# Kernel tuning notes

Hardware: AMD Instinct MI355X
Metric: run time of the kernel (lower is better)

The kernel has to match this reference:

```python
import jax, jax.numpy as jnp
import numpy as np

N = 8192
D = 256


def setup_inputs() -> dict:
    key = jax.random.key(0)
    ks = jax.random.split(key, 10)
    s = 1.0 / np.sqrt(D)
    inp = {
        "embeddings": jax.random.normal(ks[0], (N, D), dtype=jnp.float32),
        "adjacency": jax.random.randint(ks[1], (N, N), 0, 2, dtype=jnp.int32),
        "Wq": jax.random.uniform(ks[2], (D, D), jnp.float32, -s, s),
        "bq": jax.random.uniform(ks[3], (D,), jnp.float32, -s, s),
        "Wk": jax.random.uniform(ks[4], (D, D), jnp.float32, -s, s),
        "bk": jax.random.uniform(ks[5], (D,), jnp.float32, -s, s),
        "Wv": jax.random.uniform(ks[6], (D, D), jnp.float32, -s, s),
        "bv": jax.random.uniform(ks[7], (D,), jnp.float32, -s, s),
        "Wo": jax.random.uniform(ks[8], (D, D), jnp.float32, -s, s),
        "bo": jax.random.uniform(ks[9], (D,), jnp.float32, -s, s),
    }
    return inp


def reference(embeddings, adjacency, Wq, bq, Wk, bk, Wv, bv, Wo, bo):
    # Q/K/V projections (torch Linear: x @ W.T + b)
    Q = embeddings @ Wq.T + bq            # [N, D]
    K = embeddings @ Wk.T + bk            # [N, D]
    V = embeddings @ Wv.T + bv            # [N, D]
    scale = 1.0 / jnp.sqrt(jnp.asarray(D, dtype=embeddings.dtype))
    scores = (Q @ K.T) * scale            # [N, N]
    scores = jnp.where(adjacency == 0, jnp.asarray(-1e9, scores.dtype), scores)
    attn = jax.nn.softmax(scores, axis=-1)  # dropout is identity in eval mode
    context = attn @ V                    # [N, D]
    return context @ Wo.T + bo
```

## Files before the change

kernel.cpp:

```cpp
#include <hip/hip_runtime.h>
#include <hip/hip_bf16.h>


#define LOG2E 1.44269504088896340736f
#define MASKVAL -3.0e38f
#define MINIT   -1.0e38f

using f32x4 = __attribute__((ext_vector_type(4))) float;
using s16x8 = __attribute__((ext_vector_type(8))) short;
using s16x4 = __attribute__((ext_vector_type(4))) short;

__device__ __forceinline__ void gl_lds16(void* l, const void* g) {
  __builtin_amdgcn_global_load_lds(
      (const __attribute__((address_space(1))) void*)g,
      (__attribute__((address_space(3))) void*)l, 16, 0, 0);
}

__device__ __forceinline__ short f2bf(float x) {
  union { float f; unsigned u; } v; v.f = x;
  unsigned r = v.u + 0x7fffu + ((v.u >> 16) & 1u);
  return (short)(r >> 16);
}

__device__ __forceinline__ s16x8 cvt_frag(f32x4 a, f32x4 b) {
  s16x8 r;
  r[0]=f2bf(a[0]); r[1]=f2bf(a[1]); r[2]=f2bf(a[2]); r[3]=f2bf(a[3]);
  r[4]=f2bf(b[0]); r[5]=f2bf(b[1]); r[6]=f2bf(b[2]); r[7]=f2bf(b[3]);
  return r;
}

__device__ __forceinline__ f32x4 mfma16(s16x8 a, s16x8 b, f32x4 c) {
  return __builtin_amdgcn_mfma_f32_16x16x32_bf16(a, b, c, 0, 0, 0);
}

template<bool A_BF16, bool OUT_BF16, bool TRANS_OUT>
__global__ __launch_bounds__(256, 4)
void proj_kernel(const void* __restrict__ Ap, const float* __restrict__ W,
                 const float* __restrict__ bias, void* __restrict__ outp,
                 float scale)
{
  __shared__ __align__(16) char ldsA[A_BF16 ? 8192 : 16384];
  __shared__ __align__(16) char ldsB[16384];
  const int tid = threadIdx.x;
  const int lane = tid & 63, w = tid >> 6;
  const int wr = w >> 1, wc = w & 1;
  const int l15 = lane & 15, lhi = lane >> 4;
  const int m0 = blockIdx.x * 64, n0 = blockIdx.y * 64;
  const char* Ab = (const char*)Ap;
  const char* Wb = (const char*)W;

  f32x4 acc[2][2] = {};

  for (int k0 = 0; k0 < 256; k0 += 64) {
    if (A_BF16) {
#pragma unroll
      for (int i = 0; i < 2; ++i) {
        int o = tid * 16 + i * 4096;
        int row = o >> 7, inrow = o & 127;
        gl_lds16(ldsA + o, Ab + (size_t)(m0 + row) * 512 + k0 * 2 + (inrow ^ ((row & 7) << 4)));
      }
    } else {
#pragma unroll
      for (int i = 0; i < 4; ++i) {
        int o = tid * 16 + i * 4096;
        int row = o >> 8, inrow = o & 255;
        gl_lds16(ldsA + o, Ab + (size_t)(m0 + row) * 1024 + k0 * 4 + (inrow ^ ((row & 7) << 4)));
      }
    }
#pragma unroll
    for (int i = 0; i < 4; ++i) {
      int o = tid * 16 + i * 4096;
      int row = o >> 8, inrow = o & 255;
      gl_lds16(ldsB + o, Wb + (size_t)(n0 + row) * 1024 + k0 * 4 + (inrow ^ ((row & 7) << 4)));
    }
    __syncthreads();

#pragma unroll
    for (int ks = 0; ks < 2; ++ks) {
      s16x8 af[2], bfr[2];
#pragma unroll
      for (int m = 0; m < 2; ++m) {
        int row = wr * 32 + m * 16 + l15;
        if (A_BF16) {
          int c = ks * 64 + lhi * 16;
          af[m] = *(const s16x8*)(ldsA + row * 128 + (c ^ ((row & 7) << 4)));
        } else {
          int c = ks * 128 + lhi * 32;
          f32x4 lo = *(const f32x4*)(ldsA + row * 256 + (c ^ ((row & 7) << 4)));
          f32x4 hi = *(const f32x4*)(ldsA + row * 256 + ((c + 16) ^ ((row & 7) << 4)));
          af[m] = cvt_frag(lo, hi);
        }
      }
#pragma unroll
      for (int n = 0; n < 2; ++n) {
        int row = wc * 32 + n * 16 + l15;
        int c = ks * 128 + lhi * 32;
        f32x4 lo = *(const f32x4*)(ldsB + row * 256 + (c ^ ((row & 7) << 4)));
        f32x4 hi = *(const f32x4*)(ldsB + row * 256 + ((c + 16) ^ ((row & 7) << 4)));
        bfr[n] = cvt_frag(lo, hi);
      }
#pragma unroll
      for (int m = 0; m < 2; ++m)
#pragma unroll
        for (int n = 0; n < 2; ++n)
          acc[m][n] = mfma16(af[m], bfr[n], acc[m][n]);
    }
    __syncthreads();
  }

#pragma unroll
  for (int n = 0; n < 2; ++n) {
    int col = n0 + wc * 32 + n * 16 + l15;
    float bv = bias[col];
#pragma unroll
    for (int m = 0; m < 2; ++m) {
      int rbase = m0 + wr * 32 + m * 16 + lhi * 4;
      if (TRANS_OUT) {
        s16x4 pk;
#pragma unroll
        for (int r = 0; r < 4; ++r) pk[r] = f2bf((acc[m][n][r] + bv) * scale);
        *(s16x4*)((unsigned short*)outp + (size_t)col * 8192 + rbase) = pk;
      } else if (OUT_BF16) {
#pragma unroll
        for (int r = 0; r < 4; ++r)
          ((unsigned short*)outp)[(size_t)(rbase + r) * 256 + col] =
              (unsigned short)f2bf((acc[m][n][r] + bv) * scale);
      } else {
#pragma unroll
        for (int r = 0; r < 4; ++r)
          ((float*)outp)[(size_t)(rbase + r) * 256 + col] = (acc[m][n][r] + bv) * scale;
      }
    }
  }
}

template<int SPLIT, bool DIRECT, bool PACC_BF16>
__global__ __launch_bounds__(256, 2)
void attn_kernel(const unsigned short* __restrict__ Qb, const char* __restrict__ Kb,
                 const char* __restrict__ VbT, const int* __restrict__ adj,
                 void* __restrict__ pacc, float* __restrict__ pm,
                 float* __restrict__ pl, unsigned short* __restrict__ CX)
{
  __shared__ __align__(16) char ldsK[32768];
  __shared__ __align__(16) char ldsV[32768];
  __shared__ __align__(16) char ldsP[16384];
  const int tid = threadIdx.x, lane = tid & 63, w = tid >> 6;
  const int l15 = lane & 15, lhi = lane >> 4;
  const int qt = blockIdx.x / SPLIT, sp = blockIdx.x % SPLIT;
  const int q0 = qt * 128 + w * 32;
  char* myP = ldsP + w * 4096;
  const int kv_begin = sp * (8192 / SPLIT);
  const int NT = 8192 / SPLIT / 64;

  s16x8 qf[2][8];
#pragma unroll
  for (int f = 0; f < 2; ++f) {
    const unsigned short* qp = Qb + (size_t)(q0 + f * 16 + l15) * 256 + lhi * 8;
#pragma unroll
    for (int ks = 0; ks < 8; ++ks) qf[f][ks] = *(const s16x8*)(qp + ks * 32);
  }

  f32x4 ctx[2][16] = {};
  float m_run[2][4], l_run[2][4];
#pragma unroll
  for (int f = 0; f < 2; ++f)
#pragma unroll
    for (int r = 0; r < 4; ++r) { m_run[f][r] = MINIT; l_run[f][r] = 0.f; }

  for (int t = 0; t < NT; ++t) {
    const int kv0 = kv_begin + t * 64;

    {
      const char* kg = Kb + (size_t)kv0 * 512;
#pragma unroll
      for (int i = 0; i < 8; ++i) {
        int o = tid * 16 + i * 4096;
        int row = o >> 9, inrow = o & 511;
        gl_lds16(ldsK + o, kg + row * 512 + (inrow ^ ((row & 7) << 4)));
      }
#pragma unroll
      for (int i = 0; i < 8; ++i) {
        int o = tid * 16 + i * 4096;
        int row = o >> 7, inrow = o & 127;
        gl_lds16(ldsV + o, VbT + (size_t)row * 16384 + (size_t)kv0 * 2 + (inrow ^ ((row & 7) << 4)));
      }
    }

    int am[2][4][4];
#pragma unroll
    for (int f = 0; f < 2; ++f) {
      const int* ap = adj + (size_t)(q0 + f * 16 + lhi * 4) * 8192 + kv0 + l15;
#pragma unroll
      for (int r = 0; r < 4; ++r)
#pragma unroll
        for (int cg = 0; cg < 4; ++cg)
          am[f][r][cg] = ap[(size_t)r * 8192 + cg * 16];
    }

    __syncthreads();

    f32x4 sacc[2][4] = {};
    __builtin_amdgcn_s_setprio(1);
#pragma unroll
    for (int ks = 0; ks < 8; ++ks)
#pragma unroll
      for (int cg = 0; cg < 4; ++cg) {
        int row = cg * 16 + l15;
        s16x8 kf = *(const s16x8*)(ldsK + row * 512 + ((ks * 64 + lhi * 16) ^ ((row & 7) << 4)));
        sacc[0][cg] = mfma16(qf[0][ks], kf, sacc[0][cg]);
        sacc[1][cg] = mfma16(qf[1][ks], kf, sacc[1][cg]);
      }
    __builtin_amdgcn_s_setprio(0);

#pragma unroll
    for (int f = 0; f < 2; ++f)
#pragma unroll
      for (int r = 0; r < 4; ++r)
#pragma unroll
        for (int cg = 0; cg < 4; ++cg)
          if (am[f][r][cg] == 0) sacc[f][cg][r] = MASKVAL;

    float tmax[2][4];
#pragma unroll
    for (int f = 0; f < 2; ++f)
#pragma unroll
      for (int r = 0; r < 4; ++r)
        tmax[f][r] = fmaxf(fmaxf(sacc[f][0][r], sacc[f][1][r]),
                           fmaxf(sacc[f][2][r], sacc[f][3][r]));
#pragma unroll
    for (int mk = 1; mk <= 8; mk <<= 1)
#pragma unroll
      for (int f = 0; f < 2; ++f)
#pragma unroll
        for (int r = 0; r < 4; ++r)
          tmax[f][r] = fmaxf(tmax[f][r], __shfl_xor(tmax[f][r], mk, 64));

    float need = MASKVAL;
#pragma unroll
    for (int f = 0; f < 2; ++f)
#pragma unroll
      for (int r = 0; r < 4; ++r)
        need = fmaxf(need, tmax[f][r] - m_run[f][r]);
    if (!__all(need <= 8.0f)) {
#pragma unroll
      for (int f = 0; f < 2; ++f) {
        f32x4 fv;
#pragma unroll
        for (int r = 0; r < 4; ++r) {
          float mnew = fmaxf(m_run[f][r], tmax[f][r]);
          float fs = __builtin_amdgcn_exp2f((m_run[f][r] - mnew) * LOG2E);
          m_run[f][r] = mnew; l_run[f][r] *= fs; fv[r] = fs;
        }
#pragma unroll
        for (int dm = 0; dm < 16; ++dm) ctx[f][dm] *= fv;
      }
    }

#pragma unroll
    for (int f = 0; f < 2; ++f)
#pragma unroll
      for (int cg = 0; cg < 4; ++cg)
#pragma unroll
        for (int r = 0; r < 4; ++r) {
          float p = __builtin_amdgcn_exp2f((sacc[f][cg][r] - m_run[f][r]) * LOG2E);
          l_run[f][r] += p;
          int row = f * 16 + lhi * 4 + r;
          int cb = (cg * 16 + l15) * 2;
          *(short*)(myP + row * 128 + (cb ^ ((row & 7) << 4))) = f2bf(p);
        }

    __builtin_amdgcn_s_setprio(1);
#pragma unroll
    for (int ks = 0; ks < 2; ++ks) {
      s16x8 pf[2];
#pragma unroll
      for (int f = 0; f < 2; ++f) {
        int prow = f * 16 + l15;
        pf[f] = *(const s16x8*)(myP + prow * 128 + (((ks * 32 + lhi * 8) * 2) ^ ((prow & 7) << 4)));
      }
#pragma unroll
      for (int dm = 0; dm < 16; ++dm) {
        int vrow = dm * 16 + l15;
        s16x8 vf = *(const s16x8*)(ldsV + vrow * 128 + (((ks * 32 + lhi * 8) * 2) ^ ((vrow & 7) << 4)));
        ctx[0][dm] = mfma16(pf[0], vf, ctx[0][dm]);
        ctx[1][dm] = mfma16(pf[1], vf, ctx[1][dm]);
      }
    }
    __builtin_amdgcn_s_setprio(0);
    __syncthreads();
  }

#pragma unroll
  for (int mk = 1; mk <= 8; mk <<= 1)
#pragma unroll
    for (int f = 0; f < 2; ++f)
#pragma unroll
      for (int r = 0; r < 4; ++r)
        l_run[f][r] += __shfl_xor(l_run[f][r], mk, 64);

  if (DIRECT) {
#pragma unroll
    for (int f = 0; f < 2; ++f)
#pragma unroll
      for (int r = 0; r < 4; ++r) {
        float inv = 1.0f / l_run[f][r];
        size_t rowb = (size_t)(q0 + f * 16 + lhi * 4 + r) * 256 + l15;
#pragma unroll
        for (int dm = 0; dm < 16; ++dm)
          CX[rowb + dm * 16] = (unsigned short)f2bf(ctx[f][dm][r] * inv);
      }
  } else {
#pragma unroll
    for (int f = 0; f < 2; ++f)
#pragma unroll
      for (int r = 0; r < 4; ++r) {
        size_t rowb = (size_t)sp * 8192 * 256 +
                      (size_t)(q0 + f * 16 + lhi * 4 + r) * 256 + l15;
        if (PACC_BF16) {
#pragma unroll
          for (int dm = 0; dm < 16; ++dm)
            ((unsigned short*)pacc)[rowb + dm * 16] = (unsigned short)f2bf(ctx[f][dm][r]);
        } else {
#pragma unroll
          for (int dm = 0; dm < 16; ++dm)
            ((float*)pacc)[rowb + dm * 16] = ctx[f][dm][r];
        }
      }
    if (l15 == 0) {
#pragma unroll
      for (int f = 0; f < 2; ++f)
#pragma unroll
        for (int r = 0; r < 4; ++r) {
          pm[(size_t)sp * 8192 + q0 + f * 16 + lhi * 4 + r] = m_run[f][r];
          pl[(size_t)sp * 8192 + q0 + f * 16 + lhi * 4 + r] = l_run[f][r];
        }
    }
  }
}

template<bool PACC_BF16>
__global__ __launch_bounds__(256)
void combine_kernel(const void* __restrict__ pacc, const float* __restrict__ pm,
                    const float* __restrict__ pl, unsigned short* __restrict__ cx)
{
  const int row = blockIdx.x;
  const int d = threadIdx.x;
  float M = MINIT;
#pragma unroll
  for (int s = 0; s < 8; ++s) M = fmaxf(M, pm[s * 8192 + row]);
  float L = 0.f, v = 0.f;
#pragma unroll
  for (int s = 0; s < 8; ++s) {
    float ws = __builtin_amdgcn_exp2f((pm[s * 8192 + row] - M) * LOG2E);
    L += ws * pl[s * 8192 + row];
    size_t idx = (size_t)s * 8192 * 256 + (size_t)row * 256 + d;
    float pv;
    if (PACC_BF16) {
      union { unsigned u; float f; } c; c.u = (unsigned)((const unsigned short*)pacc)[idx] << 16;
      pv = c.f;
    } else {
      pv = ((const float*)pacc)[idx];
    }
    v += ws * pv;
  }
  cx[(size_t)row * 256 + d] = (unsigned short)f2bf(v / L);
}

extern "C" void kernel_launch(void* const* d_in, const int* in_sizes, int n_in,
                              void* d_out, int out_size, void* d_ws, size_t ws_size,
                              hipStream_t stream)
{
  const float* E  = (const float*)d_in[0];
  const int*  adj = (const int*)d_in[1];
  const float* Wq = (const float*)d_in[2];
  const float* bq = (const float*)d_in[3];
  const float* Wk = (const float*)d_in[4];
  const float* bk = (const float*)d_in[5];
  const float* Wv = (const float*)d_in[6];
  const float* bv = (const float*)d_in[7];
  const float* Wo = (const float*)d_in[8];
  const float* bo = (const float*)d_in[9];

  char* ws = (char*)d_ws;
  unsigned short* Qb = (unsigned short*)(ws);
  unsigned short* Kb = (unsigned short*)(ws + ((size_t)4 << 20));
  unsigned short* VT = (unsigned short*)(ws + ((size_t)8 << 20));
  unsigned short* CX = (unsigned short*)(ws + ((size_t)12 << 20));
  char* pacc = ws + ((size_t)16 << 20);

  dim3 g(128, 4), b(256);
  hipLaunchKernelGGL((proj_kernel<false, true, false>), g, b, 0, stream, E, Wq, bq, Qb, 0.0625f);
  hipLaunchKernelGGL((proj_kernel<false, true, false>), g, b, 0, stream, E, Wk, bk, Kb, 1.0f);
  hipLaunchKernelGGL((proj_kernel<false, true, true>),  g, b, 0, stream, E, Wv, bv, VT, 1.0f);

  const size_t PACC_F32_BYTES  = (size_t)8 * 8192 * 256 * 4;
  const size_t PACC_BF16_BYTES = (size_t)8 * 8192 * 256 * 2;
  const size_t PMPL = (size_t)8 * 8192 * 4;
  const size_t NEED_F32  = ((size_t)16 << 20) + PACC_F32_BYTES + 2 * PMPL;
  const size_t NEED_BF16 = ((size_t)16 << 20) + PACC_BF16_BYTES + 2 * PMPL;

  if (ws_size >= NEED_F32) {
    float* pm = (float*)(pacc + PACC_F32_BYTES);
    float* pl = pm + 8 * 8192;
    hipLaunchKernelGGL((attn_kernel<8, false, false>), dim3(512), b, 0, stream,
                       Qb, (const char*)Kb, (const char*)VT, adj, pacc, pm, pl, CX);
    hipLaunchKernelGGL((combine_kernel<false>), dim3(8192), b, 0, stream, pacc, pm, pl, CX);
  } else if (ws_size >= NEED_BF16) {
    float* pm = (float*)(pacc + PACC_BF16_BYTES);
    float* pl = pm + 8 * 8192;
    hipLaunchKernelGGL((attn_kernel<8, false, true>), dim3(512), b, 0, stream,
                       Qb, (const char*)Kb, (const char*)VT, adj, pacc, pm, pl, CX);
    hipLaunchKernelGGL((combine_kernel<true>), dim3(8192), b, 0, stream, pacc, pm, pl, CX);
  } else {
    float* pm = (float*)pacc; float* pl = pm + 8192;
    hipLaunchKernelGGL((attn_kernel<1, true, false>), dim3(64), b, 0, stream,
                       Qb, (const char*)Kb, (const char*)VT, adj, pacc, pm, pl, CX);
  }
  hipLaunchKernelGGL((proj_kernel<true, false, false>), g, b, 0, stream, CX, Wo, bo, d_out, 1.0f);
}
```

Baseline: 675.8 us.

## Repack adjacency to bitmask and fuse Q/K/V projections into one kernel

Adds a pre-pass that compresses the int32 adjacency matrix into a per-row bitmask using wave ballots. The attention kernel then reads one 64-bit word per row per tile instead of 16 scattered ints per lane, which cuts the mask traffic inside the attention loop. The three Q/K/V projections are also fused into one kernel that loads the embedding tile once and reuses it for all three weight matrices. The cost is an extra full read of the 256MB adjacency in the repack pass, plus more LDS use and lower occupancy in the fused projection.

```diff
diff --git a/kernel.cpp b/kernel.cpp
--- a/kernel.cpp
+++ b/kernel.cpp
@@ -33,45 +33,135 @@
   return __builtin_amdgcn_mfma_f32_16x16x32_bf16(a, b, c, 0, 0, 0);
 }
 
-template<bool A_BF16, bool OUT_BF16, bool TRANS_OUT>
+__global__ __launch_bounds__(256)
+void repack_kernel(const int* __restrict__ adj, unsigned long long* __restrict__ bm)
+{
+  const int row = blockIdx.x;
+  const int w = threadIdx.x >> 6, lane = threadIdx.x & 63;
+  const int* src = adj + (size_t)row * 8192 + w * 2048;
+  unsigned long long* dst = bm + (size_t)row * 128 + w * 32;
+#pragma unroll 4
+  for (int it = 0; it < 32; ++it) {
+    int x = src[it * 64 + lane];
+    unsigned long long b = __ballot(x != 0);
+    if (lane == 0) dst[it] = b;
+  }
+}
+
+__global__ __launch_bounds__(256, 2)
+void qkv_kernel(const float* __restrict__ E,
+                const float* __restrict__ Wq, const float* __restrict__ bq,
+                const float* __restrict__ Wk, const float* __restrict__ bk,
+                const float* __restrict__ Wv, const float* __restrict__ bv,
+                unsigned short* __restrict__ Qb, unsigned short* __restrict__ Kb,
+                unsigned short* __restrict__ VT)
+{
+  __shared__ __align__(16) char ldsA[16384];
+  __shared__ __align__(16) char ldsB[3][16384];
+  const int tid = threadIdx.x;
+  const int lane = tid & 63, w = tid >> 6;
+  const int wr = w >> 1, wc = w & 1;
+  const int l15 = lane & 15, lhi = lane >> 4;
+  const int m0 = blockIdx.x * 64, n0 = blockIdx.y * 64;
+  const float* Ws[3] = {Wq, Wk, Wv};
+
+  f32x4 acc[3][2][2] = {};
+
+  for (int k0 = 0; k0 < 256; k0 += 64) {
+#pragma unroll
+    for (int i = 0; i < 4; ++i) {
+      int o = tid * 16 + i * 4096;
+      int row = o >> 8, inrow = o & 255;
+      gl_lds16(ldsA + o, (const char*)E + (size_t)(m0 + row) * 1024 + k0 * 4 + (inrow ^ ((row & 7) << 4)));
+    }
+#pragma unroll
+    for (int mtx = 0; mtx < 3; ++mtx)
+#pragma unroll
+      for (int i = 0; i < 4; ++i) {
+        int o = tid * 16 + i * 4096;
+        int row = o >> 8, inrow = o & 255;
+        gl_lds16(ldsB[mtx] + o, (const char*)Ws[mtx] + (size_t)(n0 + row) * 1024 + k0 * 4 + (inrow ^ ((row & 7) << 4)));
+      }
+    __syncthreads();
+
+#pragma unroll
+    for (int ks = 0; ks < 2; ++ks) {
+      s16x8 af[2];
+#pragma unroll
+      for (int m = 0; m < 2; ++m) {
+        int row = wr * 32 + m * 16 + l15;
+        int c = ks * 128 + lhi * 32;
+        f32x4 lo = *(const f32x4*)(ldsA + row * 256 + (c ^ ((row & 7) << 4)));
+        f32x4 hi = *(const f32x4*)(ldsA + row * 256 + ((c + 16) ^ ((row & 7) << 4)));
+        af[m] = cvt_frag(lo, hi);
+      }
+#pragma unroll
+      for (int mtx = 0; mtx < 3; ++mtx) {
+        s16x8 bfr[2];
+#pragma unroll
+        for (int n = 0; n < 2; ++n) {
+          int row = wc * 32 + n * 16 + l15;
+          int c = ks * 128 + lhi * 32;
+          f32x4 lo = *(const f32x4*)(ldsB[mtx] + row * 256 + (c ^ ((row & 7) << 4)));
+          f32x4 hi = *(const f32x4*)(ldsB[mtx] + row * 256 + ((c + 16) ^ ((row & 7) << 4)));
+          bfr[n] = cvt_frag(lo, hi);
+        }
+#pragma unroll
+        for (int m = 0; m < 2; ++m)
+#pragma unroll
+          for (int n = 0; n < 2; ++n)
+            acc[mtx][m][n] = mfma16(af[m], bfr[n], acc[mtx][m][n]);
+      }
+    }
+    __syncthreads();
+  }
+
+#pragma unroll
+  for (int n = 0; n < 2; ++n) {
+    int col = n0 + wc * 32 + n * 16 + l15;
+    float bvq = bq[col], bvk = bk[col], bvv = bv[col];
+#pragma unroll
+    for (int m = 0; m < 2; ++m) {
+      int rbase = m0 + wr * 32 + m * 16 + lhi * 4;
+#pragma unroll
+      for (int r = 0; r < 4; ++r) {
+        Qb[(size_t)(rbase + r) * 256 + col] = (unsigned short)f2bf((acc[0][m][n][r] + bvq) * 0.0625f);
+        Kb[(size_t)(rbase + r) * 256 + col] = (unsigned short)f2bf(acc[1][m][n][r] + bvk);
+      }
+      s16x4 pk;
+#pragma unroll
+      for (int r = 0; r < 4; ++r) pk[r] = f2bf(acc[2][m][n][r] + bvv);
+      *(s16x4*)(VT + (size_t)col * 8192 + rbase) = pk;
+    }
+  }
+}
+
 __global__ __launch_bounds__(256, 4)
-void proj_kernel(const void* __restrict__ Ap, const float* __restrict__ W,
-                 const float* __restrict__ bias, void* __restrict__ outp,
-                 float scale)
-{
-  __shared__ __align__(16) char ldsA[A_BF16 ? 8192 : 16384];
+void projo_kernel(const unsigned short* __restrict__ Ap, const float* __restrict__ W,
+                  const float* __restrict__ bias, float* __restrict__ outp)
+{
+  __shared__ __align__(16) char ldsA[8192];
   __shared__ __align__(16) char ldsB[16384];
   const int tid = threadIdx.x;
   const int lane = tid & 63, w = tid >> 6;
   const int wr = w >> 1, wc = w & 1;
   const int l15 = lane & 15, lhi = lane >> 4;
   const int m0 = blockIdx.x * 64, n0 = blockIdx.y * 64;
-  const char* Ab = (const char*)Ap;
-  const char* Wb = (const char*)W;
 
   f32x4 acc[2][2] = {};
 
   for (int k0 = 0; k0 < 256; k0 += 64) {
-    if (A_BF16) {
-#pragma unroll
-      for (int i = 0; i < 2; ++i) {
-        int o = tid * 16 + i * 4096;
-        int row = o >> 7, inrow = o & 127;
-        gl_lds16(ldsA + o, Ab + (size_t)(m0 + row) * 512 + k0 * 2 + (inrow ^ ((row & 7) << 4)));
-      }
-    } else {
-#pragma unroll
-      for (int i = 0; i < 4; ++i) {
-        int o = tid * 16 + i * 4096;
-        int row = o >> 8, inrow = o & 255;
-        gl_lds16(ldsA + o, Ab + (size_t)(m0 + row) * 1024 + k0 * 4 + (inrow ^ ((row & 7) << 4)));
-      }
+#pragma unroll
+    for (int i = 0; i < 2; ++i) {
+      int o = tid * 16 + i * 4096;
+      int row = o >> 7, inrow = o & 127;
+      gl_lds16(ldsA + o, (const char*)Ap + (size_t)(m0 + row) * 512 + k0 * 2 + (inrow ^ ((row & 7) << 4)));
     }
 #pragma unroll
     for (int i = 0; i < 4; ++i) {
       int o = tid * 16 + i * 4096;
       int row = o >> 8, inrow = o & 255;
-      gl_lds16(ldsB + o, Wb + (size_t)(n0 + row) * 1024 + k0 * 4 + (inrow ^ ((row & 7) << 4)));
+      gl_lds16(ldsB + o, (const char*)W + (size_t)(n0 + row) * 1024 + k0 * 4 + (inrow ^ ((row & 7) << 4)));
     }
     __syncthreads();
 
@@ -81,15 +171,8 @@
 #pragma unroll
       for (int m = 0; m < 2; ++m) {
         int row = wr * 32 + m * 16 + l15;
-        if (A_BF16) {
-          int c = ks * 64 + lhi * 16;
-          af[m] = *(const s16x8*)(ldsA + row * 128 + (c ^ ((row & 7) << 4)));
-        } else {
-          int c = ks * 128 + lhi * 32;
-          f32x4 lo = *(const f32x4*)(ldsA + row * 256 + (c ^ ((row & 7) << 4)));
-          f32x4 hi = *(const f32x4*)(ldsA + row * 256 + ((c + 16) ^ ((row & 7) << 4)));
-          af[m] = cvt_frag(lo, hi);
-        }
+        int c = ks * 64 + lhi * 16;
+        af[m] = *(const s16x8*)(ldsA + row * 128 + (c ^ ((row & 7) << 4)));
       }
 #pragma unroll
       for (int n = 0; n < 2; ++n) {
@@ -115,21 +198,9 @@
 #pragma unroll
     for (int m = 0; m < 2; ++m) {
       int rbase = m0 + wr * 32 + m * 16 + lhi * 4;
-      if (TRANS_OUT) {
-        s16x4 pk;
-#pragma unroll
-        for (int r = 0; r < 4; ++r) pk[r] = f2bf((acc[m][n][r] + bv) * scale);
-        *(s16x4*)((unsigned short*)outp + (size_t)col * 8192 + rbase) = pk;
-      } else if (OUT_BF16) {
-#pragma unroll
-        for (int r = 0; r < 4; ++r)
-          ((unsigned short*)outp)[(size_t)(rbase + r) * 256 + col] =
-              (unsigned short)f2bf((acc[m][n][r] + bv) * scale);
-      } else {
-#pragma unroll
-        for (int r = 0; r < 4; ++r)
-          ((float*)outp)[(size_t)(rbase + r) * 256 + col] = (acc[m][n][r] + bv) * scale;
-      }
+#pragma unroll
+      for (int r = 0; r < 4; ++r)
+        outp[(size_t)(rbase + r) * 256 + col] = acc[m][n][r] + bv;
     }
   }
 }
@@ -137,7 +208,7 @@
 template<int SPLIT, bool DIRECT, bool PACC_BF16>
 __global__ __launch_bounds__(256, 2)
 void attn_kernel(const unsigned short* __restrict__ Qb, const char* __restrict__ Kb,
-                 const char* __restrict__ VbT, const int* __restrict__ adj,
+                 const char* __restrict__ VbT, const unsigned long long* __restrict__ bm,
                  void* __restrict__ pacc, float* __restrict__ pm,
                  float* __restrict__ pl, unsigned short* __restrict__ CX)
 {
@@ -186,15 +257,12 @@
       }
     }
 
-    int am[2][4][4];
+    unsigned long long bmv[2][4];
 #pragma unroll
     for (int f = 0; f < 2; ++f) {
-      const int* ap = adj + (size_t)(q0 + f * 16 + lhi * 4) * 8192 + kv0 + l15;
-#pragma unroll
-      for (int r = 0; r < 4; ++r)
-#pragma unroll
-        for (int cg = 0; cg < 4; ++cg)
-          am[f][r][cg] = ap[(size_t)r * 8192 + cg * 16];
+      const unsigned long long* bp = bm + (size_t)(q0 + f * 16 + lhi * 4) * 128 + (kv0 >> 6);
+#pragma unroll
+      for (int r = 0; r < 4; ++r) bmv[f][r] = bp[(size_t)r * 128];
     }
 
     __syncthreads();
@@ -215,10 +283,12 @@
 #pragma unroll
     for (int f = 0; f < 2; ++f)
 #pragma unroll
-      for (int r = 0; r < 4; ++r)
+      for (int r = 0; r < 4; ++r) {
+        unsigned long long ms = bmv[f][r] >> l15;
 #pragma unroll
         for (int cg = 0; cg < 4; ++cg)
-          if (am[f][r][cg] == 0) sacc[f][cg][r] = MASKVAL;
+          if (!((unsigned)(ms >> (cg * 16)) & 1u)) sacc[f][cg][r] = MASKVAL;
+      }
 
     float tmax[2][4];
 #pragma unroll
@@ -386,35 +456,36 @@
   unsigned short* Kb = (unsigned short*)(ws + ((size_t)4 << 20));
   unsigned short* VT = (unsigned short*)(ws + ((size_t)8 << 20));
   unsigned short* CX = (unsigned short*)(ws + ((size_t)12 << 20));
-  char* pacc = ws + ((size_t)16 << 20);
-
-  dim3 g(128, 4), b(256);
-  hipLaunchKernelGGL((proj_kernel<false, true, false>), g, b, 0, stream, E, Wq, bq, Qb, 0.0625f);
-  hipLaunchKernelGGL((proj_kernel<false, true, false>), g, b, 0, stream, E, Wk, bk, Kb, 1.0f);
-  hipLaunchKernelGGL((proj_kernel<false, true, true>),  g, b, 0, stream, E, Wv, bv, VT, 1.0f);
+  unsigned long long* bm = (unsigned long long*)(ws + ((size_t)16 << 20));
+  char* pacc = ws + ((size_t)24 << 20);
+
+  dim3 b(256);
+  hipLaunchKernelGGL(repack_kernel, dim3(8192), b, 0, stream, adj, bm);
+  hipLaunchKernelGGL(qkv_kernel, dim3(128, 4), b, 0, stream,
+                     E, Wq, bq, Wk, bk, Wv, bv, Qb, Kb, VT);
 
   const size_t PACC_F32_BYTES  = (size_t)8 * 8192 * 256 * 4;
   const size_t PACC_BF16_BYTES = (size_t)8 * 8192 * 256 * 2;
   const size_t PMPL = (size_t)8 * 8192 * 4;
-  const size_t NEED_F32  = ((size_t)16 << 20) + PACC_F32_BYTES + 2 * PMPL;
-  const size_t NEED_BF16 = ((size_t)16 << 20) + PACC_BF16_BYTES + 2 * PMPL;
+  const size_t NEED_F32  = ((size_t)24 << 20) + PACC_F32_BYTES + 2 * PMPL;
+  const size_t NEED_BF16 = ((size_t)24 << 20) + PACC_BF16_BYTES + 2 * PMPL;
 
   if (ws_size >= NEED_F32) {
     float* pm = (float*)(pacc + PACC_F32_BYTES);
     float* pl = pm + 8 * 8192;
     hipLaunchKernelGGL((attn_kernel<8, false, false>), dim3(512), b, 0, stream,
-                       Qb, (const char*)Kb, (const char*)VT, adj, pacc, pm, pl, CX);
+                       Qb, (const char*)Kb, (const char*)VT, bm, pacc, pm, pl, CX);
     hipLaunchKernelGGL((combine_kernel<false>), dim3(8192), b, 0, stream, pacc, pm, pl, CX);
   } else if (ws_size >= NEED_BF16) {
     float* pm = (float*)(pacc + PACC_BF16_BYTES);
     float* pl = pm + 8 * 8192;
     hipLaunchKernelGGL((attn_kernel<8, false, true>), dim3(512), b, 0, stream,
-                       Qb, (const char*)Kb, (const char*)VT, adj, pacc, pm, pl, CX);
+                       Qb, (const char*)Kb, (const char*)VT, bm, pacc, pm, pl, CX);
     hipLaunchKernelGGL((combine_kernel<true>), dim3(8192), b, 0, stream, pacc, pm, pl, CX);
   } else {
     float* pm = (float*)pacc; float* pl = pm + 8192;
     hipLaunchKernelGGL((attn_kernel<1, true, false>), dim3(64), b, 0, stream,
-                       Qb, (const char*)Kb, (const char*)VT, adj, pacc, pm, pl, CX);
-  }
-  hipLaunchKernelGGL((proj_kernel<true, false, false>), g, b, 0, stream, CX, Wo, bo, d_out, 1.0f);
-}
+                       Qb, (const char*)Kb, (const char*)VT, bm, pacc, pm, pl, CX);
+  }
+  hipLaunchKernelGGL(projo_kernel, dim3(128, 4), b, 0, stream, CX, Wo, bo, (float*)d_out);
+}
```

Result: slower. 717.0 us (+6.1%).
